# Kernel optimization log

Hardware: AMD Instinct MI355X
Metric: run time of the kernel (lower is better)

Reference implementation:

```python
import jax, jax.numpy as jnp
import numpy as np

B, S, R = 8192, 256, 8192  # gas cells, species, reactions


def setup_inputs() -> dict:
    key = jax.random.key(0)
    ks = jax.random.split(key, 10)
    abundances = jax.random.uniform(ks[0], (B, S), jnp.float32, 1e-12, 1.0)
    temperature = jax.random.uniform(ks[1], (B,), jnp.float32, 10.0, 300.0)
    cr_rate = jax.random.uniform(ks[2], (B,), jnp.float32, 0.1, 10.0)
    fuv_rate = jax.random.uniform(ks[3], (B,), jnp.float32, 0.1, 10.0)
    time = jnp.zeros((B,), jnp.float32)  # unused by the RHS, kept for signature parity
    incidence = jax.random.normal(ks[4], (S, R), jnp.float32)  # stoichiometry matrix
    alpha = jax.random.uniform(ks[5], (R,), jnp.float32, 1e-12, 1e-9)
    beta = jax.random.normal(ks[6], (R,), jnp.float32) * 0.5
    gamma = jax.random.uniform(ks[7], (R,), jnp.float32, 0.0, 100.0)
    # species index or S (== out-of-bounds sentinel -> fill_value 1.0, i.e. <2 reactants)
    reactant_multipliers = jax.random.randint(ks[8], (R, 2), 0, S + 1, jnp.int32)
    rtype = jax.random.randint(ks[9], (R,), 0, 3, jnp.int32)  # 0: Arrhenius, 1: CR, 2: FUV
    return {
        'time': time, 'abundances': abundances, 'temperature': temperature,
        'cr_rate': cr_rate, 'fuv_rate': fuv_rate, 'incidence': incidence,
        'alpha': alpha, 'beta': beta, 'gamma': gamma,
        'reactant_multipliers': reactant_multipliers, 'rtype': rtype,
    }


def _get_rates(temperature, cr_rate, fuv_rate, alpha, beta, gamma, rtype):
    # JNetwork.get_rates: hstack of per-reaction rate terms -> (B, R)
    T = temperature[:, None]                                      # (B, 1)
    k_arr = alpha * jnp.exp(beta * jnp.log(T / 300.0) - gamma / T)  # Arrhenius
    k_cr = alpha * cr_rate[:, None]                               # cosmic-ray driven
    k_fuv = alpha * jnp.exp(-gamma) * fuv_rate[:, None]           # FUV photorate
    return jnp.where(rtype == 0, k_arr, jnp.where(rtype == 1, k_cr, k_fuv))


def reference(time, abundances, temperature, cr_rate, fuv_rate,
              incidence, alpha, beta, gamma, reactant_multipliers, rtype):
    rates = _get_rates(temperature, cr_rate, fuv_rate, alpha, beta, gamma, rtype)
    # multiply_rates_by_abundance: gather reactant abundances (mode='drop',
    # fill_value=1.0) and reduce with a product over the 2 reactant slots.
    ones_col = jnp.ones((abundances.shape[0], 1), abundances.dtype)
    ab_pad = jnp.concatenate([abundances, ones_col], axis=1)      # (B, S+1), col S == 1.0
    prod = ab_pad[:, reactant_multipliers[:, 0]] * ab_pad[:, reactant_multipliers[:, 1]]  # (B, R)
    flux = rates * prod                                           # (B, R)
    # incidence @ rates, batched: (S, R) x (B, R) -> (B, S)
    return jnp.einsum('sr,br->bs', incidence, flux)
```

## Files before the change

kernel.cpp:

```cpp
#include <hip/hip_runtime.h>
#include <stdint.h>

typedef __bf16 bf16;
typedef __bf16 bf16x8 __attribute__((ext_vector_type(8)));
typedef float  f32x4  __attribute__((ext_vector_type(4)));

#if __has_builtin(__builtin_amdgcn_exp2f)
#define EXP2F(x) __builtin_amdgcn_exp2f(x)
#else
#define EXP2F(x) exp2f(x)
#endif

#define GLD_LDS16(g, l)                                                                    \
  __builtin_amdgcn_global_load_lds((const __attribute__((address_space(1))) uint32_t*)(g), \
                                   (__attribute__((address_space(3))) uint32_t*)(l), 16, 0, 0)

constexpr int Bn = 8192, Sn = 256, Rn = 8192;
constexpr int BM = 64, BK = 32, KP = 4;
constexpr int KLEN = Rn / KP;
constexpr int NC = KLEN / BK;

__global__ __launch_bounds__(256) void prep_all(
    const float* __restrict__ inc, bf16* __restrict__ incb,
    const float* __restrict__ alpha, const float* __restrict__ beta,
    const float* __restrict__ gam, const int* __restrict__ rm, const int* __restrict__ rtype,
    float4* __restrict__ params, const float* __restrict__ temp,
    const float* __restrict__ cr, const float* __restrict__ fuv, float4* __restrict__ perb) {
  const int g = blockIdx.x, tid = threadIdx.x;
  size_t e = ((size_t)g * 256 + tid) * 8;
  int n = (int)(e >> 13);
  int kpos = (int)(e & 8191);
  int sw = (n >> 1) & 3;
  int src = (kpos & ~31) | (((((kpos >> 3) & 3)) ^ sw) << 3);
  const float* sp = inc + ((size_t)n << 13) + src;
  float4 v0 = *(const float4*)(sp);
  float4 v1 = *(const float4*)(sp + 4);
  bf16x8 o;
  o[0] = (bf16)v0.x; o[1] = (bf16)v0.y; o[2] = (bf16)v0.z; o[3] = (bf16)v0.w;
  o[4] = (bf16)v1.x; o[5] = (bf16)v1.y; o[6] = (bf16)v1.z; o[7] = (bf16)v1.w;
  *(bf16x8*)(incb + e) = o;
  if (g < 32) {
    int r = g * 256 + tid;
    float a = alpha[r], be = beta[r], gm = gam[r];
    int ty = rtype[r];
    int i0 = rm[2 * r], i1 = rm[2 * r + 1];
    float A = a, P = 0.0f, Q = 0.0f;
    if (ty == 0) { P = be; Q = gm; }
    else if (ty == 2) { A = a * expf(-gm); }
    uint32_t bits = (uint32_t)i0 | ((uint32_t)i1 << 10) | ((uint32_t)ty << 20);
    params[r] = make_float4(A, P, Q, __uint_as_float(bits));
  } else if (g < 64) {
    int b = (g - 32) * 256 + tid;
    float T = temp[b];
    perb[b] = make_float4(log2f(T * (1.0f / 300.0f)), 1.4426950408889634f / T, cr[b], fuv[b]);
  }
}

__global__ __launch_bounds__(256, 2) void flux_gemm(
    const float* __restrict__ abund, const float4* __restrict__ perb,
    const float4* __restrict__ params, const bf16* __restrict__ incb,
    float* __restrict__ partial) {
  __shared__ bf16 ab_lds[257 * 64];
  __shared__ bf16 inc_lds[2][256 * BK];
  __shared__ bf16 flux_lds[2][64 * BK];

  const int tid  = threadIdx.x;
  const int lane = tid & 63;
  const int w    = tid >> 6;
  const int x   = blockIdx.x & 7;
  const int jb  = blockIdx.x >> 3;
  const int kp  = x & 3;
  const int m0g = (jb * 2 + (x >> 2)) * BM;
  const int kstart = kp * KLEN;
  const int r16 = lane & 15, q = lane >> 4;
  const int sw16 = (r16 >> 1) & 3;
  const int fsw  = w ^ ((lane >> 1) & 3);

#pragma unroll
  for (int i = 0; i < 4; ++i) {
    int rrow = w * 64 + i * 16 + (lane >> 2);
    const bf16* gp = incb + (size_t)rrow * Rn + kstart + (lane & 3) * 8;
    GLD_LDS16(gp, inc_lds[0] + (w * 64 + i * 16) * BK);
  }

  {
    int bsub = tid >> 2;
    int scol = (tid & 3) * 64;
    const float* rowp = abund + (size_t)(m0g + bsub) * Sn + scol;
#pragma unroll
    for (int j = 0; j < 16; ++j) {
      float4 v = *(const float4*)(rowp + j * 4);
      int s = scol + j * 4;
      ab_lds[(s + 0) * 64 + bsub] = (bf16)v.x;
      ab_lds[(s + 1) * 64 + bsub] = (bf16)v.y;
      ab_lds[(s + 2) * 64 + bsub] = (bf16)v.z;
      ab_lds[(s + 3) * 64 + bsub] = (bf16)v.w;
    }
    if (tid < 64) ab_lds[256 * 64 + tid] = (bf16)1.0f;
  }

  float4 pb = perb[m0g + lane];
  const float l2t = pb.x, itv = pb.y, crv = pb.z, fuvv = pb.w;

  __syncthreads();

  {
    const float4* pw = params + kstart + w * 8;
    bf16x8 fv;
#pragma unroll
    for (int j = 0; j < 8; ++j) {
      float4 pr = pw[j];
      uint32_t bits = __float_as_uint(pr.w);
      int i0 = bits & 1023, i1 = (bits >> 10) & 1023, ms = (int)(bits >> 20);
      float a0 = (float)ab_lds[i0 * 64 + lane];
      float a1 = (float)ab_lds[i1 * 64 + lane];
      float v = EXP2F(pr.y * l2t - pr.z * itv);
      float mult = (ms == 1) ? crv : ((ms == 2) ? fuvv : 1.0f);
      fv[j] = (bf16)(pr.x * v * mult * a0 * a1);
    }
    *(bf16x8*)(flux_lds[0] + lane * BK + fsw * 8) = fv;
  }

  f32x4 acc[4][4];
#pragma unroll
  for (int i = 0; i < 4; ++i)
#pragma unroll
    for (int j = 0; j < 4; ++j) acc[i][j] = (f32x4)0.0f;

  for (int c = 0; c < NC; ++c) {
    const int cur = c & 1, nxt = cur ^ 1;
    __syncthreads();

    bf16x8 af[4], bfr[4];
#pragma unroll
    for (int mt = 0; mt < 4; ++mt)
      af[mt] = *(const bf16x8*)(flux_lds[cur] + (mt * 16 + r16) * BK + (q ^ sw16) * 8);
#pragma unroll
    for (int nt = 0; nt < 4; ++nt)
      bfr[nt] = *(const bf16x8*)(inc_lds[cur] + (w * 64 + nt * 16 + r16) * BK + (q ^ sw16) * 8);

    if (c + 1 < NC) {
      const int kb = kstart + (c + 1) * BK;
#pragma unroll
      for (int i = 0; i < 4; ++i) {
        int rrow = w * 64 + i * 16 + (lane >> 2);
        const bf16* gp = incb + (size_t)rrow * Rn + kb + (lane & 3) * 8;
        GLD_LDS16(gp, inc_lds[nxt] + (w * 64 + i * 16) * BK);
      }
      const float4* pw = params + kb + w * 8;
      bf16x8 fv;
#pragma unroll
      for (int j = 0; j < 8; ++j) {
        float4 pr = pw[j];
        uint32_t bits = __float_as_uint(pr.w);
        int i0 = bits & 1023, i1 = (bits >> 10) & 1023, ms = (int)(bits >> 20);
        float a0 = (float)ab_lds[i0 * 64 + lane];
        float a1 = (float)ab_lds[i1 * 64 + lane];
        float v = EXP2F(pr.y * l2t - pr.z * itv);
        float mult = (ms == 1) ? crv : ((ms == 2) ? fuvv : 1.0f);
        fv[j] = (bf16)(pr.x * v * mult * a0 * a1);
      }
      *(bf16x8*)(flux_lds[nxt] + lane * BK + fsw * 8) = fv;
    }

#pragma unroll
    for (int mt = 0; mt < 4; ++mt)
#pragma unroll
      for (int nt = 0; nt < 4; ++nt)
        acc[mt][nt] = __builtin_amdgcn_mfma_f32_16x16x32_bf16(af[mt], bfr[nt], acc[mt][nt], 0, 0, 0);
  }

  float* pout = partial + (size_t)kp * Bn * Sn;
#pragma unroll
  for (int mt = 0; mt < 4; ++mt)
#pragma unroll
    for (int nt = 0; nt < 4; ++nt) {
      int col = w * 64 + nt * 16 + r16;
      int row = m0g + mt * 16 + q * 4;
#pragma unroll
      for (int rg = 0; rg < 4; ++rg)
        pout[(size_t)(row + rg) * Sn + col] = acc[mt][nt][rg];
    }
}

__global__ __launch_bounds__(256) void reduce_k(const float* __restrict__ partial,
                                               float* __restrict__ out) {
  size_t i = ((size_t)blockIdx.x * 256 + threadIdx.x) * 4;
  constexpr size_t NS = (size_t)Bn * Sn;
  float4 a = *(const float4*)(partial + i);
  float4 b = *(const float4*)(partial + NS + i);
  float4 c = *(const float4*)(partial + 2 * NS + i);
  float4 d = *(const float4*)(partial + 3 * NS + i);
  float4 r;
  r.x = (a.x + b.x) + (c.x + d.x);
  r.y = (a.y + b.y) + (c.y + d.y);
  r.z = (a.z + b.z) + (c.z + d.z);
  r.w = (a.w + b.w) + (c.w + d.w);
  *(float4*)(out + i) = r;
}

extern "C" void kernel_launch(void* const* d_in, const int* in_sizes, int n_in,
                              void* d_out, int out_size, void* d_ws, size_t ws_size,
                              hipStream_t stream) {
  const float* abund = (const float*)d_in[1];
  const float* temp  = (const float*)d_in[2];
  const float* cr    = (const float*)d_in[3];
  const float* fuv   = (const float*)d_in[4];
  const float* inc   = (const float*)d_in[5];
  const float* alpha = (const float*)d_in[6];
  const float* beta  = (const float*)d_in[7];
  const float* gam   = (const float*)d_in[8];
  const int*   rm    = (const int*)d_in[9];
  const int*   rty   = (const int*)d_in[10];
  float* out = (float*)d_out;

  float4* params  = (float4*)d_ws;
  float4* perb    = params + Rn;
  bf16*   incb    = (bf16*)(perb + Bn);
  float*  partial = (float*)(incb + (size_t)Sn * Rn);

  prep_all<<<1024, 256, 0, stream>>>(inc, incb, alpha, beta, gam, rm, rty,
                                     params, temp, cr, fuv, perb);
  flux_gemm<<<(Bn / BM) * KP, 256, 0, stream>>>(abund, perb, params, incb, partial);
  reduce_k<<<(Bn * Sn) / 1024, 256, 0, stream>>>(partial, out);
}
```

Baseline: 173.1 us.

## Load incidence fragments directly from global and fold rate multipliers into log domain

The incidence B-operand is no longer staged through LDS via global_load_lds. Each wave reads its MFMA fragments straight from the unswizzled bf16 incidence copy in global memory, which removes the inc_lds buffers and lowers LDS use. The rate computation now stores log2 of alpha, cr and fuv so that each flux becomes a single exp2 of a fused argument, and the per-reaction packed bits are made wave-uniform with readfirstlane. The costs are lower-precision __log2f calls, a reliance on the cache for reuse of incidence across blocks, and global-load latency that is no longer prefetched ahead of use.

```diff
diff --git a/kernel.cpp b/kernel.cpp
--- a/kernel.cpp
+++ b/kernel.cpp
@@ -10,10 +10,6 @@
 #else
 #define EXP2F(x) exp2f(x)
 #endif
-
-#define GLD_LDS16(g, l)                                                                    \
-  __builtin_amdgcn_global_load_lds((const __attribute__((address_space(1))) uint32_t*)(g), \
-                                   (__attribute__((address_space(3))) uint32_t*)(l), 16, 0, 0)
 
 constexpr int Bn = 8192, Sn = 256, Rn = 8192;
 constexpr int BM = 64, BK = 32, KP = 4;
@@ -28,13 +24,8 @@
     const float* __restrict__ cr, const float* __restrict__ fuv, float4* __restrict__ perb) {
   const int g = blockIdx.x, tid = threadIdx.x;
   size_t e = ((size_t)g * 256 + tid) * 8;
-  int n = (int)(e >> 13);
-  int kpos = (int)(e & 8191);
-  int sw = (n >> 1) & 3;
-  int src = (kpos & ~31) | (((((kpos >> 3) & 3)) ^ sw) << 3);
-  const float* sp = inc + ((size_t)n << 13) + src;
-  float4 v0 = *(const float4*)(sp);
-  float4 v1 = *(const float4*)(sp + 4);
+  float4 v0 = *(const float4*)(inc + e);
+  float4 v1 = *(const float4*)(inc + e + 4);
   bf16x8 o;
   o[0] = (bf16)v0.x; o[1] = (bf16)v0.y; o[2] = (bf16)v0.z; o[3] = (bf16)v0.w;
   o[4] = (bf16)v1.x; o[5] = (bf16)v1.y; o[6] = (bf16)v1.z; o[7] = (bf16)v1.w;
@@ -44,15 +35,17 @@
     float a = alpha[r], be = beta[r], gm = gam[r];
     int ty = rtype[r];
     int i0 = rm[2 * r], i1 = rm[2 * r + 1];
-    float A = a, P = 0.0f, Q = 0.0f;
+    float P = 0.0f, Q = 0.0f;
+    float l2A = __log2f(a);
     if (ty == 0) { P = be; Q = gm; }
-    else if (ty == 2) { A = a * expf(-gm); }
+    else if (ty == 2) { l2A = fmaf(-gm, 1.4426950408889634f, l2A); }
     uint32_t bits = (uint32_t)i0 | ((uint32_t)i1 << 10) | ((uint32_t)ty << 20);
-    params[r] = make_float4(A, P, Q, __uint_as_float(bits));
+    params[r] = make_float4(l2A, P, Q, __uint_as_float(bits));
   } else if (g < 64) {
     int b = (g - 32) * 256 + tid;
     float T = temp[b];
-    perb[b] = make_float4(log2f(T * (1.0f / 300.0f)), 1.4426950408889634f / T, cr[b], fuv[b]);
+    perb[b] = make_float4(__log2f(T * (1.0f / 300.0f)), 1.4426950408889634f / T,
+                          __log2f(cr[b]), __log2f(fuv[b]));
   }
 }
 
@@ -61,7 +54,6 @@
     const float4* __restrict__ params, const bf16* __restrict__ incb,
     float* __restrict__ partial) {
   __shared__ bf16 ab_lds[257 * 64];
-  __shared__ bf16 inc_lds[2][256 * BK];
   __shared__ bf16 flux_lds[2][64 * BK];
 
   const int tid  = threadIdx.x;
@@ -75,13 +67,6 @@
   const int r16 = lane & 15, q = lane >> 4;
   const int sw16 = (r16 >> 1) & 3;
   const int fsw  = w ^ ((lane >> 1) & 3);
-
-#pragma unroll
-  for (int i = 0; i < 4; ++i) {
-    int rrow = w * 64 + i * 16 + (lane >> 2);
-    const bf16* gp = incb + (size_t)rrow * Rn + kstart + (lane & 3) * 8;
-    GLD_LDS16(gp, inc_lds[0] + (w * 64 + i * 16) * BK);
-  }
 
   {
     int bsub = tid >> 2;
@@ -100,26 +85,28 @@
   }
 
   float4 pb = perb[m0g + lane];
-  const float l2t = pb.x, itv = pb.y, crv = pb.z, fuvv = pb.w;
+  const float l2t = pb.x, nitv = -pb.y, l2cr = pb.z, l2fuv = pb.w;
 
-  __syncthreads();
-
-  {
-    const float4* pw = params + kstart + w * 8;
+  auto flux_tile = [&](int kb, int buf) {
+    const float4* pw = params + kb + w * 8;
     bf16x8 fv;
 #pragma unroll
     for (int j = 0; j < 8; ++j) {
       float4 pr = pw[j];
-      uint32_t bits = __float_as_uint(pr.w);
-      int i0 = bits & 1023, i1 = (bits >> 10) & 1023, ms = (int)(bits >> 20);
+      uint32_t bits = __builtin_amdgcn_readfirstlane(__float_as_uint(pr.w));
+      int i0 = (int)(bits & 1023), i1 = (int)((bits >> 10) & 1023), ms = (int)(bits >> 20);
       float a0 = (float)ab_lds[i0 * 64 + lane];
       float a1 = (float)ab_lds[i1 * 64 + lane];
-      float v = EXP2F(pr.y * l2t - pr.z * itv);
-      float mult = (ms == 1) ? crv : ((ms == 2) ? fuvv : 1.0f);
-      fv[j] = (bf16)(pr.x * v * mult * a0 * a1);
+      float lm = (ms == 1) ? l2cr : ((ms == 2) ? l2fuv : 0.0f);
+      float arg = fmaf(pr.y, l2t, fmaf(pr.z, nitv, pr.x + lm));
+      fv[j] = (bf16)(EXP2F(arg) * (a0 * a1));
     }
-    *(bf16x8*)(flux_lds[0] + lane * BK + fsw * 8) = fv;
-  }
+    *(bf16x8*)(flux_lds[buf] + lane * BK + fsw * 8) = fv;
+  };
+
+  __syncthreads();
+
+  flux_tile(kstart, 0);
 
   f32x4 acc[4][4];
 #pragma unroll
@@ -127,8 +114,10 @@
 #pragma unroll
     for (int j = 0; j < 4; ++j) acc[i][j] = (f32x4)0.0f;
 
+  const bf16* bptr = incb + (size_t)(w * 64 + r16) * Rn + kstart + q * 8;
+
   for (int c = 0; c < NC; ++c) {
-    const int cur = c & 1, nxt = cur ^ 1;
+    const int cur = c & 1;
     __syncthreads();
 
     bf16x8 af[4], bfr[4];
@@ -137,31 +126,9 @@
       af[mt] = *(const bf16x8*)(flux_lds[cur] + (mt * 16 + r16) * BK + (q ^ sw16) * 8);
 #pragma unroll
     for (int nt = 0; nt < 4; ++nt)
-      bfr[nt] = *(const bf16x8*)(inc_lds[cur] + (w * 64 + nt * 16 + r16) * BK + (q ^ sw16) * 8);
+      bfr[nt] = *(const bf16x8*)(bptr + (size_t)nt * 16 * Rn + c * BK);
 
-    if (c + 1 < NC) {
-      const int kb = kstart + (c + 1) * BK;
-#pragma unroll
-      for (int i = 0; i < 4; ++i) {
-        int rrow = w * 64 + i * 16 + (lane >> 2);
-        const bf16* gp = incb + (size_t)rrow * Rn + kb + (lane & 3) * 8;
-        GLD_LDS16(gp, inc_lds[nxt] + (w * 64 + i * 16) * BK);
-      }
-      const float4* pw = params + kb + w * 8;
-      bf16x8 fv;
-#pragma unroll
-      for (int j = 0; j < 8; ++j) {
-        float4 pr = pw[j];
-        uint32_t bits = __float_as_uint(pr.w);
-        int i0 = bits & 1023, i1 = (bits >> 10) & 1023, ms = (int)(bits >> 20);
-        float a0 = (float)ab_lds[i0 * 64 + lane];
-        float a1 = (float)ab_lds[i1 * 64 + lane];
-        float v = EXP2F(pr.y * l2t - pr.z * itv);
-        float mult = (ms == 1) ? crv : ((ms == 2) ? fuvv : 1.0f);
-        fv[j] = (bf16)(pr.x * v * mult * a0 * a1);
-      }
-      *(bf16x8*)(flux_lds[nxt] + lane * BK + fsw * 8) = fv;
-    }
+    if (c + 1 < NC) flux_tile(kstart + (c + 1) * BK, cur ^ 1);
 
 #pragma unroll
     for (int mt = 0; mt < 4; ++mt)
```

Result: slower. 236.6 us (+36.7%).

## Sort reactions by type so flux tiles skip exp and per-element type selects

Applied to the files above, without the earlier changes.

A new single-block kernel builds a permutation that groups reactions by rate type. The incidence matrix and per-reaction params are written in that permuted order, so most 8-reaction chunks in the GEMM hold one type and can take a branch-free path. CR/FUV chunks then skip the exp entirely, and log2(alpha) is folded into the Arrhenius exponent so each element costs one exp2 plus FMAs. Params are read through readfirstlane so they become scalar, and MFMA issue gets raised priority. The cost is an extra launch and an index-gathered read of the incidence matrix during prep, in place of the vectorised float4 loads.

```diff
diff --git a/kernel.cpp b/kernel.cpp
--- a/kernel.cpp
+++ b/kernel.cpp
@@ -20,39 +20,79 @@
 constexpr int KLEN = Rn / KP;
 constexpr int NC = KLEN / BK;
 
+__global__ __launch_bounds__(256) void build_perm(const int* __restrict__ rtype,
+                                                  int* __restrict__ perm,
+                                                  int* __restrict__ inv) {
+  __shared__ int c0[256], c1[256], c2[256];
+  const int t = threadIdx.x;
+  const int base = t * 32;
+  int ty[32];
+  int l0 = 0, l1 = 0, l2 = 0;
+#pragma unroll
+  for (int i = 0; i < 32; ++i) {
+    int v = rtype[base + i];
+    ty[i] = v;
+    l0 += (v == 0); l1 += (v == 1); l2 += (v == 2);
+  }
+  c0[t] = l0; c1[t] = l1; c2[t] = l2;
+  __syncthreads();
+  for (int off = 1; off < 256; off <<= 1) {
+    int a = (t >= off) ? c0[t - off] : 0;
+    int b = (t >= off) ? c1[t - off] : 0;
+    int c = (t >= off) ? c2[t - off] : 0;
+    __syncthreads();
+    c0[t] += a; c1[t] += b; c2[t] += c;
+    __syncthreads();
+  }
+  const int tot0 = c0[255], tot1 = c1[255];
+  int o0 = c0[t] - l0;
+  int o1 = tot0 + c1[t] - l1;
+  int o2 = tot0 + tot1 + c2[t] - l2;
+#pragma unroll
+  for (int i = 0; i < 32; ++i) {
+    int v = ty[i];
+    int pos = (v == 0) ? o0++ : ((v == 1) ? o1++ : o2++);
+    perm[pos] = base + i;
+    inv[base + i] = pos;
+  }
+}
+
 __global__ __launch_bounds__(256) void prep_all(
     const float* __restrict__ inc, bf16* __restrict__ incb,
     const float* __restrict__ alpha, const float* __restrict__ beta,
     const float* __restrict__ gam, const int* __restrict__ rm, const int* __restrict__ rtype,
     float4* __restrict__ params, const float* __restrict__ temp,
-    const float* __restrict__ cr, const float* __restrict__ fuv, float4* __restrict__ perb) {
+    const float* __restrict__ cr, const float* __restrict__ fuv, float4* __restrict__ perb,
+    const int* __restrict__ perm, const int* __restrict__ inv) {
   const int g = blockIdx.x, tid = threadIdx.x;
   size_t e = ((size_t)g * 256 + tid) * 8;
   int n = (int)(e >> 13);
   int kpos = (int)(e & 8191);
   int sw = (n >> 1) & 3;
   int src = (kpos & ~31) | (((((kpos >> 3) & 3)) ^ sw) << 3);
-  const float* sp = inc + ((size_t)n << 13) + src;
-  float4 v0 = *(const float4*)(sp);
-  float4 v1 = *(const float4*)(sp + 4);
+  const int* pp = perm + src;
+  const float* rowp = inc + ((size_t)n << 13);
   bf16x8 o;
-  o[0] = (bf16)v0.x; o[1] = (bf16)v0.y; o[2] = (bf16)v0.z; o[3] = (bf16)v0.w;
-  o[4] = (bf16)v1.x; o[5] = (bf16)v1.y; o[6] = (bf16)v1.z; o[7] = (bf16)v1.w;
+#pragma unroll
+  for (int i = 0; i < 8; ++i) o[i] = (bf16)rowp[pp[i]];
   *(bf16x8*)(incb + e) = o;
   if (g < 32) {
     int r = g * 256 + tid;
     float a = alpha[r], be = beta[r], gm = gam[r];
     int ty = rtype[r];
     int i0 = rm[2 * r], i1 = rm[2 * r + 1];
-    float A = a, P = 0.0f, Q = 0.0f;
-    if (ty == 0) { P = be; Q = gm; }
-    else if (ty == 2) { A = a * expf(-gm); }
+    float x, P = 0.0f, Q = 0.0f;
+    if (ty == 0) { x = __log2f(a); P = be; Q = gm; }
+    else if (ty == 1) { x = a; }
+    else { x = a * expf(-gm); }
     uint32_t bits = (uint32_t)i0 | ((uint32_t)i1 << 10) | ((uint32_t)ty << 20);
-    params[r] = make_float4(A, P, Q, __uint_as_float(bits));
+    float4 pv = make_float4(x, P, Q, __uint_as_float(bits));
+    params[inv[r]] = pv;
   } else if (g < 64) {
     int b = (g - 32) * 256 + tid;
     float T = temp[b];
-    perb[b] = make_float4(log2f(T * (1.0f / 300.0f)), 1.4426950408889634f / T, cr[b], fuv[b]);
+    perb[b] = make_float4(__log2f(T * (1.0f / 300.0f)), 1.4426950408889634f / T,
+                          cr[b], fuv[b]);
   }
 }
 
@@ -67,6 +107,7 @@
   const int tid  = threadIdx.x;
   const int lane = tid & 63;
   const int w    = tid >> 6;
+  const int ws   = __builtin_amdgcn_readfirstlane(w);
   const int x   = blockIdx.x & 7;
   const int jb  = blockIdx.x >> 3;
   const int kp  = x & 3;
@@ -100,26 +141,56 @@
   }
 
   float4 pb = perb[m0g + lane];
-  const float l2t = pb.x, itv = pb.y, crv = pb.z, fuvv = pb.w;
+  const float l2t = pb.x, nitv = -pb.y, crv = pb.z, fuvv = pb.w;
+
+  auto flux_tile = [&](int kb, int buf) {
+    const float4* pw = params + kb + ws * 8;
+    float4 pr[8];
+#pragma unroll
+    for (int j = 0; j < 8; ++j) pr[j] = pw[j];
+    uint32_t b0 = __builtin_amdgcn_readfirstlane(__float_as_uint(pr[0].w));
+    uint32_t b7 = __builtin_amdgcn_readfirstlane(__float_as_uint(pr[7].w));
+    uint32_t t0 = b0 >> 20, t7 = b7 >> 20;
+    bf16x8 fv;
+    if (t0 == 0 && t7 == 0) {
+#pragma unroll
+      for (int j = 0; j < 8; ++j) {
+        uint32_t bits = __builtin_amdgcn_readfirstlane(__float_as_uint(pr[j].w));
+        int i0 = (int)(bits & 1023), i1 = (int)((bits >> 10) & 1023);
+        float a0 = (float)ab_lds[i0 * 64 + lane];
+        float a1 = (float)ab_lds[i1 * 64 + lane];
+        float v = EXP2F(fmaf(pr[j].y, l2t, fmaf(pr[j].z, nitv, pr[j].x)));
+        fv[j] = (bf16)(v * (a0 * a1));
+      }
+    } else if (t0 == t7) {
+      float mv = (t0 == 1) ? crv : fuvv;
+#pragma unroll
+      for (int j = 0; j < 8; ++j) {
+        uint32_t bits = __builtin_amdgcn_readfirstlane(__float_as_uint(pr[j].w));
+        int i0 = (int)(bits & 1023), i1 = (int)((bits >> 10) & 1023);
+        float a0 = (float)ab_lds[i0 * 64 + lane];
+        float a1 = (float)ab_lds[i1 * 64 + lane];
+        fv[j] = (bf16)((pr[j].x * mv) * (a0 * a1));
+      }
+    } else {
+#pragma unroll
+      for (int j = 0; j < 8; ++j) {
+        uint32_t bits = __builtin_amdgcn_readfirstlane(__float_as_uint(pr[j].w));
+        int i0 = (int)(bits & 1023), i1 = (int)((bits >> 10) & 1023), ms = (int)(bits >> 20);
+        float a0 = (float)ab_lds[i0 * 64 + lane];
+        float a1 = (float)ab_lds[i1 * 64 + lane];
+        float ve = EXP2F(fmaf(pr[j].y, l2t, fmaf(pr[j].z, nitv, pr[j].x)));
+        float vm = pr[j].x * ((ms == 1) ? crv : fuvv);
+        float v = (ms == 0) ? ve : vm;
+        fv[j] = (bf16)(v * (a0 * a1));
+      }
+    }
+    *(bf16x8*)(flux_lds[buf] + lane * BK + fsw * 8) = fv;
+  };
 
   __syncthreads();
 
-  {
-    const float4* pw = params + kstart + w * 8;
-    bf16x8 fv;
-#pragma unroll
-    for (int j = 0; j < 8; ++j) {
-      float4 pr = pw[j];
-      uint32_t bits = __float_as_uint(pr.w);
-      int i0 = bits & 1023, i1 = (bits >> 10) & 1023, ms = (int)(bits >> 20);
-      float a0 = (float)ab_lds[i0 * 64 + lane];
-      float a1 = (float)ab_lds[i1 * 64 + lane];
-      float v = EXP2F(pr.y * l2t - pr.z * itv);
-      float mult = (ms == 1) ? crv : ((ms == 2) ? fuvv : 1.0f);
-      fv[j] = (bf16)(pr.x * v * mult * a0 * a1);
-    }
-    *(bf16x8*)(flux_lds[0] + lane * BK + fsw * 8) = fv;
-  }
+  flux_tile(kstart, 0);
 
   f32x4 acc[4][4];
 #pragma unroll
@@ -147,27 +218,16 @@
         const bf16* gp = incb + (size_t)rrow * Rn + kb + (lane & 3) * 8;
         GLD_LDS16(gp, inc_lds[nxt] + (w * 64 + i * 16) * BK);
       }
-      const float4* pw = params + kb + w * 8;
-      bf16x8 fv;
-#pragma unroll
-      for (int j = 0; j < 8; ++j) {
-        float4 pr = pw[j];
-        uint32_t bits = __float_as_uint(pr.w);
-        int i0 = bits & 1023, i1 = (bits >> 10) & 1023, ms = (int)(bits >> 20);
-        float a0 = (float)ab_lds[i0 * 64 + lane];
-        float a1 = (float)ab_lds[i1 * 64 + lane];
-        float v = EXP2F(pr.y * l2t - pr.z * itv);
-        float mult = (ms == 1) ? crv : ((ms == 2) ? fuvv : 1.0f);
-        fv[j] = (bf16)(pr.x * v * mult * a0 * a1);
-      }
-      *(bf16x8*)(flux_lds[nxt] + lane * BK + fsw * 8) = fv;
-    }
-
+      flux_tile(kb, nxt);
+    }
+
+    __builtin_amdgcn_s_setprio(1);
 #pragma unroll
     for (int mt = 0; mt < 4; ++mt)
 #pragma unroll
       for (int nt = 0; nt < 4; ++nt)
         acc[mt][nt] = __builtin_amdgcn_mfma_f32_16x16x32_bf16(af[mt], bfr[nt], acc[mt][nt], 0, 0, 0);
+    __builtin_amdgcn_s_setprio(0);
   }
 
   float* pout = partial + (size_t)kp * Bn * Sn;
@@ -218,9 +278,12 @@
   float4* perb    = params + Rn;
   bf16*   incb    = (bf16*)(perb + Bn);
   float*  partial = (float*)(incb + (size_t)Sn * Rn);
-
+  int*    perm    = (int*)partial;
+  int*    inv     = perm + Rn;
+
+  build_perm<<<1, 256, 0, stream>>>(rty, perm, inv);
   prep_all<<<1024, 256, 0, stream>>>(inc, incb, alpha, beta, gam, rm, rty,
-                                     params, temp, cr, fuv, perb);
+                                     params, temp, cr, fuv, perb, perm, inv);
   flux_gemm<<<(Bn / BM) * KP, 256, 0, stream>>>(abund, perb, params, incb, partial);
   reduce_k<<<(Bn * Sn) / 1024, 256, 0, stream>>>(partial, out);
 }
```

Result: faster. 167.6 us (-3.2%).
